# Kernel optimization log

Hardware: AMD Instinct MI355X
Metric: run time of the kernel (lower is better)

## Reference

```python
import jax, jax.numpy as jnp
import numpy as np
from jax.scipy.special import logsumexp

L, B, C, H = 1024, 256, 96, 768
STD = (1.0 / C) ** 0.5


def setup_inputs() -> dict:
    key = jax.random.key(0)
    ks = jax.random.split(key, 8)
    emit = jax.random.normal(ks[0], (L, B, C), dtype=jnp.float32)
    hidden = jax.random.normal(ks[1], (B, H), dtype=jnp.float32)
    target = jax.random.randint(ks[2], (L, B), 0, C)
    # variable sentence lengths in [L//2, L]; mask[0] is always True
    lens = jax.random.randint(ks[3], (B,), L // 2, L + 1)
    mask = jnp.arange(L)[:, None] < lens[None, :]
    Wt = jax.random.normal(ks[4], (C * C, H), dtype=jnp.float32) * STD
    bt = jnp.zeros((C * C,), dtype=jnp.float32)
    Ws = jax.random.normal(ks[5], (C, H), dtype=jnp.float32) * STD
    bs = jnp.zeros((C,), dtype=jnp.float32)
    We = jax.random.normal(ks[6], (C, H), dtype=jnp.float32) * STD
    be = jnp.zeros((C,), dtype=jnp.float32)
    return {"emit": emit, "hidden": hidden, "target": target, "mask": mask,
            "Wt": Wt, "bt": bt, "Ws": Ws, "bs": bs, "We": We, "be": be}


def _crf_loss(emit, hidden, target, mask, Wt, bt, Ws, bs, We, be):
    l, b, c = emit.shape
    trans = (hidden @ Wt.T + bt).reshape(b, c, c)          # [B, prev, next]
    t_start = hidden @ Ws.T + bs                           # [B, C]
    t_end = hidden @ We.T + be                             # [B, C]

    # ---- log partition (forward algorithm), sequential scan over time ----
    def step(log_alpha, xs):
        emit_i, mask_i = xs                                # [B,C], [B]
        # scores[b,p,n] = log_alpha[b,p] + trans[b,p,n] + emit_i[b,n]
        new = logsumexp(log_alpha[:, :, None] + trans + emit_i[:, None, :], axis=1)
        log_alpha = jnp.where(mask_i[:, None], new, log_alpha)
        return log_alpha, None

    log_alpha0 = emit[0] + t_start
    log_alpha, _ = jax.lax.scan(step, log_alpha0, (emit[1:], mask[1:]))
    log_z = logsumexp(log_alpha + t_end, axis=1).sum()

    # ---- gold path score ----
    bidx = jnp.arange(b)
    tr_sc = trans[bidx[None, :], target[:-1], target[1:]]          # [L-1, B]
    emit_sc = jnp.take_along_axis(emit, target[:, :, None], axis=2)[:, :, 0]  # [L, B]
    scores = emit_sc.at[1:].add(tr_sc)
    score = jnp.sum(scores * mask.astype(emit.dtype))
    ends = mask.sum(axis=0) - 1                                    # [B]
    last_tag = target[ends, bidx]
    score = score + t_start[bidx, target[0]].sum() + t_end[bidx, last_tag].sum()

    return (log_z - score) / b


def reference(emit, hidden, target, mask, Wt, bt, Ws, bs, We, be):
    return _crf_loss(emit, hidden, target, mask, Wt, bt, Ws, bs, We, be)
```

## Files before the change

### kernel.cpp

```cpp
#include <hip/hip_runtime.h>
#include <hip/hip_bf16.h>
#include <stdint.h>

#define LL 1024
#define BB 256
#define CC 96
#define HH 768
#define NW 9216
#define NTOT 9408
#define SEGS 8
#define SEGLEN 128
#define CHPB 15

typedef __attribute__((ext_vector_type(4))) float floatx4;
typedef __attribute__((ext_vector_type(2))) float floatx2;
typedef __attribute__((ext_vector_type(8))) short short8;

#define KAPPA 0x1p-16f
#define NEG_LOG_KAPPA 11.090354888959125f

__device__ __forceinline__ unsigned short f2bf(float f) {
  uint32_t u = __float_as_uint(f);
  return (unsigned short)((u + 0x7FFFu + ((u >> 16) & 1u)) >> 16);
}

#define GA_LD 40

__global__ __launch_bounds__(256) void gemm_mfma(
    const float* __restrict__ hidden, const float* __restrict__ Wt,
    const float* __restrict__ Ws, const float* __restrict__ We,
    const float* __restrict__ bt, const float* __restrict__ bs,
    const float* __restrict__ be, float* __restrict__ trans,
    float* __restrict__ tstart, float* __restrict__ tend) {
  __shared__ __align__(16) unsigned short As[128 * GA_LD];
  __shared__ __align__(16) unsigned short Bs[128 * GA_LD];
  const int t = threadIdx.x;
  const int lane = t & 63, wid = t >> 6;
  const int wm = wid >> 1, wn = wid & 1;
  const int l15 = lane & 15, qd = lane >> 4;
  const int m0 = blockIdx.y * 128, n0 = blockIdx.x * 128;
  const int srow = t >> 1, shalf = t & 1;

  floatx4 acc[4][4];
#pragma unroll
  for (int i = 0; i < 4; ++i)
#pragma unroll
    for (int j = 0; j < 4; ++j) acc[i][j] = (floatx4){0.f, 0.f, 0.f, 0.f};

  const int r = n0 + srow;
  const float* bsrc = (r < NW)        ? Wt + (size_t)r * HH
                      : (r < NW + CC) ? Ws + (size_t)(r - NW) * HH
                      : (r < NTOT)    ? We + (size_t)(r - NW - CC) * HH
                                      : nullptr;
  const float* asrc = hidden + (size_t)(m0 + srow) * HH;
  const int sidx = srow * GA_LD + shalf * 16;

  for (int k0 = 0; k0 < HH; k0 += 32) {
    __syncthreads();
    {
      const float4* s4 = (const float4*)(asrc + k0 + shalf * 16);
      uint32_t w[8];
#pragma unroll
      for (int u = 0; u < 4; ++u) {
        float4 v = s4[u];
        w[2 * u] = (uint32_t)f2bf(v.x) | ((uint32_t)f2bf(v.y) << 16);
        w[2 * u + 1] = (uint32_t)f2bf(v.z) | ((uint32_t)f2bf(v.w) << 16);
      }
      *(uint4*)&As[sidx] = make_uint4(w[0], w[1], w[2], w[3]);
      *(uint4*)&As[sidx + 8] = make_uint4(w[4], w[5], w[6], w[7]);
    }
    {
      uint32_t w[8];
      if (bsrc) {
        const float4* s4 = (const float4*)(bsrc + k0 + shalf * 16);
#pragma unroll
        for (int u = 0; u < 4; ++u) {
          float4 v = s4[u];
          w[2 * u] = (uint32_t)f2bf(v.x) | ((uint32_t)f2bf(v.y) << 16);
          w[2 * u + 1] = (uint32_t)f2bf(v.z) | ((uint32_t)f2bf(v.w) << 16);
        }
      } else {
#pragma unroll
        for (int u = 0; u < 8; ++u) w[u] = 0u;
      }
      *(uint4*)&Bs[sidx] = make_uint4(w[0], w[1], w[2], w[3]);
      *(uint4*)&Bs[sidx + 8] = make_uint4(w[4], w[5], w[6], w[7]);
    }
    __syncthreads();
    short8 af[4], bf[4];
#pragma unroll
    for (int i = 0; i < 4; ++i)
      af[i] = *(const short8*)&As[(64 * wm + 16 * i + l15) * GA_LD + qd * 8];
#pragma unroll
    for (int j = 0; j < 4; ++j)
      bf[j] = *(const short8*)&Bs[(64 * wn + 16 * j + l15) * GA_LD + qd * 8];
#pragma unroll
    for (int i = 0; i < 4; ++i)
#pragma unroll
      for (int j = 0; j < 4; ++j)
        acc[i][j] = __builtin_amdgcn_mfma_f32_16x16x32_bf16(af[i], bf[j],
                                                            acc[i][j], 0, 0, 0);
  }

#pragma unroll
  for (int j = 0; j < 4; ++j) {
    int n = n0 + 64 * wn + 16 * j + l15;
    if (n >= NTOT) continue;
    float bv;
    float* dst;
    int ldo;
    if (n < NW) {
      bv = bt[n]; dst = trans + n; ldo = NW;
    } else if (n < NW + CC) {
      bv = bs[n - NW]; dst = tstart + (n - NW); ldo = CC;
    } else {
      bv = be[n - NW - CC]; dst = tend + (n - NW - CC); ldo = CC;
    }
#pragma unroll
    for (int i = 0; i < 4; ++i)
#pragma unroll
      for (int rr = 0; rr < 4; ++rr) {
        int m = m0 + 64 * wm + 16 * i + 4 * qd + rr;
        dst[(size_t)m * ldo] = acc[i][j][rr] + bv;
      }
  }
}

__device__ __forceinline__ float wredf(float v) {
#pragma unroll
  for (int m = 32; m >= 1; m >>= 1) v += __shfl_xor(v, m);
  return v;
}
__device__ __forceinline__ int wredi(int v) {
#pragma unroll
  for (int m = 32; m >= 1; m >>= 1) v += __shfl_xor(v, m);
  return v;
}
__device__ __forceinline__ float bcast0(float x) {
  return __uint_as_float(__builtin_amdgcn_readfirstlane(__float_as_uint(x)));
}
__device__ __forceinline__ int get_len(const void* mask, int b, int l) {
  int cnt = 0;
  unsigned w0 = *(const unsigned*)mask;
  if (w0 == 1u) {
    const int* m32 = (const int*)mask;
    for (int i = l; i < LL; i += 64) cnt += (m32[i * BB + b] != 0);
  } else if (w0 == 0x01010101u) {
    const unsigned char* m8 = (const unsigned char*)mask;
    for (int i = l; i < LL; i += 64) cnt += (m8[i * BB + b] != 0);
  } else {
    const float* mf = (const float*)mask;
    for (int i = l; i < LL; i += 64) cnt += (mf[i * BB + b] != 0.f);
  }
  return wredi(cnt);
}

__global__ __launch_bounds__(64, 2) void crf_chain(
    const float* __restrict__ emit, const void* __restrict__ mask,
    const float* __restrict__ trans, const float* __restrict__ tstart,
    float* __restrict__ xvec, float* __restrict__ lsc) {
  const int cid = blockIdx.x;
  const int b = cid / CHPB;
  const int k = cid - CHPB * b;
  const bool isfw = (k < SEGS);
  const int seg = isfw ? k : (k - (SEGS - 1));
  const int l = threadIdx.x;
  const int pr = l >> 1, s = l & 1;

  __shared__ __align__(16) float ebuf[2][8][CC];
  __shared__ __align__(16) float u_lds[CC];

  const int len = get_len(mask, b, l);
  const int lo = seg * SEGLEN + 1;
  const int hi = min((seg + 1) * SEGLEN, len - 1);
  float* xout = xvec + (size_t)cid * CC;
  if (hi < lo) {
    xout[l] = 1.f;
    if (l < 32) xout[l + 64] = 1.f;
    if (l == 0) lsc[cid] = 0.f;
    return;
  }
  const int n = hi - lo + 1;

  const float* tb = trans + (size_t)b * (CC * CC);
  floatx2 T2[3][24];
  if (isfw) {
#pragma unroll
    for (int j = 0; j < 24; ++j) {
      const float* r0 = tb + (48 * s + 2 * j) * CC + 3 * pr;
      const float* r1 = r0 + CC;
#pragma unroll
      for (int o = 0; o < 3; ++o)
        T2[o][j] = (floatx2){__expf(r0[o]), __expf(r1[o])};
    }
  } else {
#pragma unroll
    for (int o = 0; o < 3; ++o) {
      const float* row = tb + (3 * pr + o) * CC + 48 * s;
#pragma unroll
      for (int j = 0; j < 24; ++j)
        T2[o][j] = (floatx2){__expf(row[2 * j]), __expf(row[2 * j + 1])};
    }
  }

  const float4* e4 = (const float4*)emit;
  const int eoff = 3 * pr + 2 * s;
  float L = 0.f, pv = 1.f;

#define STAGE_CHUNK(baserow, slot)                                        \
  {                                                                       \
    _Pragma("unroll") for (int u = 0; u < 3; ++u) {                       \
      int v = l + 64 * u;                                                 \
      int rw = v / 24, c4 = v - 24 * rw;                                  \
      float4 vv = e4[(((baserow) + rw) * BB + b) * 24 + c4];              \
      floatx4 o = {__expf(vv.x) * KAPPA, __expf(vv.y) * KAPPA,            \
                   __expf(vv.z) * KAPPA, __expf(vv.w) * KAPPA};           \
      *(floatx4*)&ebuf[slot][rw][c4 * 4] = o;                             \
    }                                                                     \
  }

#define INNER_DOT(a0, a1, a2)                                             \
  float a0, a1, a2;                                                       \
  {                                                                       \
    const floatx4* up = (const floatx4*)&u_lds[48 * s];                   \
    floatx2 A0 = {0.f, 0.f}, B0 = {0.f, 0.f};                             \
    floatx2 A1 = {0.f, 0.f}, B1 = {0.f, 0.f};                             \
    floatx2 A2 = {0.f, 0.f}, B2 = {0.f, 0.f};                             \
    _Pragma("unroll") for (int j4 = 0; j4 < 12; ++j4) {                   \
      floatx4 U = up[j4];                                                 \
      floatx2 lo2 = {U.x, U.y}, hi2 = {U.z, U.w};                         \
      A0 += lo2 * T2[0][2 * j4]; B0 += hi2 * T2[0][2 * j4 + 1];           \
      A1 += lo2 * T2[1][2 * j4]; B1 += hi2 * T2[1][2 * j4 + 1];           \
      A2 += lo2 * T2[2][2 * j4]; B2 += hi2 * T2[2][2 * j4 + 1];           \
    }                                                                     \
    floatx2 S0 = A0 + B0, S1 = A1 + B1, S2 = A2 + B2;                     \
    a0 = S0.x + S0.y; a1 = S1.x + S1.y; a2 = S2.x + S2.y;                 \
    a0 += __shfl_xor(a0, 1);                                              \
    a1 += __shfl_xor(a1, 1);                                              \
    a2 += __shfl_xor(a2, 1);                                              \
  }

  if (isfw) {
    const int base0 = lo & ~7;
    STAGE_CHUNK(base0, (base0 >> 3) & 1);
    if (seg == 0) {
      float a00 = emit[(size_t)b * CC] + tstart[b * CC];
      L = a00;
      float v = emit[(size_t)b * CC + l] + tstart[b * CC + l];
      u_lds[l] = __expf(v - a00);
      if (l < 32) {
        int c2 = l + 64;
        float v2 = emit[(size_t)b * CC + c2] + tstart[b * CC + c2];
        u_lds[c2] = __expf(v2 - a00);
      }
    } else {
      u_lds[l] = 1.f;
      if (l < 32) u_lds[l + 64] = 1.f;
    }
    asm volatile("" ::: "memory");
    int jj = 1;
    for (int i = lo; i <= hi; ++i, ++jj) {
      if ((i & 7) == 0) {
        STAGE_CHUNK(i, (i >> 3) & 1);
        asm volatile("" ::: "memory");
      }
      float invP = 1.f;
      if ((jj & 3) == 0) { invP = 1.0f / pv; L += __logf(pv); }
      INNER_DOT(a0, a1, a2);
      floatx2 E = *(const floatx2*)&ebuf[(i >> 3) & 1][i & 7][eoff];
      float o0 = a0 * E.x * invP;
      if (((jj + 1) & 3) == 0) pv = bcast0(o0);
      if (s == 0) {
        floatx2 wv = {o0, a1 * E.y * invP};
        *(floatx2*)&u_lds[3 * pr] = wv;
      } else {
        u_lds[3 * pr + 2] = a2 * E.x * invP;
      }
      asm volatile("" ::: "memory");
    }
  } else {
    const int cb = hi & ~7;
    STAGE_CHUNK(cb, (cb >> 3) & 1);
    asm volatile("" ::: "memory");
    u_lds[l] = ebuf[(hi >> 3) & 1][hi & 7][l];
    if (l < 32) u_lds[l + 64] = ebuf[(hi >> 3) & 1][hi & 7][l + 64];
    asm volatile("" ::: "memory");
    int jj = 1;
    for (int i = hi; i >= lo; --i, ++jj) {
      if ((i & 7) == 0 && i > lo) {
        STAGE_CHUNK(i - 8, ((i >> 3) & 1) ^ 1);
        asm volatile("" ::: "memory");
      }
      float invP = 1.f;
      if ((jj & 3) == 0) { invP = 1.0f / pv; L += __logf(pv); }
      INNER_DOT(a0, a1, a2);
      floatx2 E = (i > lo)
          ? *(const floatx2*)&ebuf[((i - 1) >> 3) & 1][(i - 1) & 7][eoff]
          : (floatx2){1.f, 1.f};
      float o0 = a0 * E.x * invP;
      if (((jj + 1) & 3) == 0) pv = bcast0(o0);
      if (s == 0) {
        floatx2 wv = {o0, a1 * E.y * invP};
        *(floatx2*)&u_lds[3 * pr] = wv;
      } else {
        u_lds[3 * pr + 2] = a2 * E.x * invP;
      }
      asm volatile("" ::: "memory");
    }
  }

  asm volatile("" ::: "memory");
  xout[l] = u_lds[l];
  if (l < 32) xout[l + 64] = u_lds[l + 64];
  if (l == 0) lsc[cid] = L + (float)n * NEG_LOG_KAPPA;
}

__global__ __launch_bounds__(64) void crf_compose(
    const float* __restrict__ emit, const int* __restrict__ target,
    const void* __restrict__ mask, const float* __restrict__ trans,
    const float* __restrict__ tstart, const float* __restrict__ tend,
    const float* __restrict__ xvec, const float* __restrict__ lsc,
    float* __restrict__ out) {
  const int b = blockIdx.x;
  const int l = threadIdx.x;
  const int len = get_len(mask, b, l);

  float Lam = lsc[b * CHPB + 0];
  const float* xcur = xvec + (size_t)(b * CHPB + 0) * CC;
  for (int s2 = 1; s2 < SEGS; ++s2) {
    if (s2 * SEGLEN + 1 > len - 1) break;
    const float* bh = xvec + (size_t)(b * CHPB + (SEGS - 1) + s2) * CC;
    const float* ah = xvec + (size_t)(b * CHPB + s2) * CC;
    float pn = bh[l] * xcur[l];
    float pd = bh[l];
    if (l < 32) {
      pn += bh[l + 64] * xcur[l + 64];
      pd += bh[l + 64];
    }
    float num = wredf(pn), den = wredf(pd);
    Lam += __logf(num / den) + lsc[b * CHPB + s2];
    xcur = ah;
  }
  float zp = xcur[l] * __expf(tend[b * CC + l]);
  if (l < 32) zp += xcur[l + 64] * __expf(tend[b * CC + l + 64]);
  float logz = Lam + __logf(wredf(zp));

  const float* tb = trans + (size_t)b * (CC * CC);
  float sc = 0.f;
  for (int i = l; i < len; i += 64) {
    int tg = target[i * BB + b];
    sc += emit[((size_t)i * BB + b) * CC + tg];
    if (i >= 1) sc += tb[target[(i - 1) * BB + b] * CC + tg];
  }
  float score = wredf(sc);
  if (l == 0) {
    score += tstart[b * CC + target[b]] +
             tend[b * CC + target[(len - 1) * BB + b]];
    atomicAdd(out, (logz - score) * (1.0f / 256.0f));
  }
}

extern "C" void kernel_launch(void* const* d_in, const int* in_sizes, int n_in,
                              void* d_out, int out_size, void* d_ws, size_t ws_size,
                              hipStream_t stream) {
  const float* emit = (const float*)d_in[0];
  const float* hidden = (const float*)d_in[1];
  const int* target = (const int*)d_in[2];
  const void* mask = d_in[3];
  const float* Wt = (const float*)d_in[4];
  const float* bt = (const float*)d_in[5];
  const float* Ws = (const float*)d_in[6];
  const float* bs = (const float*)d_in[7];
  const float* We = (const float*)d_in[8];
  const float* be = (const float*)d_in[9];

  float* trans_ws = (float*)d_ws;
  float* ts_ws = trans_ws + (size_t)BB * CC * CC;
  float* te_ws = ts_ws + (size_t)BB * CC;
  float* xvec = te_ws + (size_t)BB * CC;
  float* lsc = xvec + (size_t)BB * CHPB * CC;

  hipMemsetAsync(d_out, 0, sizeof(float), stream);

  gemm_mfma<<<dim3((NTOT + 127) / 128, 2), 256, 0, stream>>>(
      hidden, Wt, Ws, We, bt, bs, be, trans_ws, ts_ws, te_ws);

  crf_chain<<<BB * CHPB, 64, 0, stream>>>(emit, mask, trans_ws, ts_ws, xvec, lsc);

  crf_compose<<<BB, 64, 0, stream>>>(emit, target, mask, trans_ws, ts_ws, te_ws,
                                     xvec, lsc, (float*)d_out);
}
```

Before: 389.6 us.

## Interleave two independent chain segments per wavefront in crf_chain

Each 64-thread block now runs two independent segment recurrences (A and B) in lockstep, sharing the exp-transformed transition registers, so the latency of one segment's dot and LDS round trip can overlap with the other's. The grid drops from 15 blocks per batch row to 8, and launch bounds move from 2 to 1 waves per EU to make room for the extra state. Segments whose length exceeds the shorter partner run in tail loops. The cost is fewer concurrent waves and serial tails when the two segment lengths differ.

```diff
diff --git a/kernel.cpp b/kernel.cpp
--- a/kernel.cpp
+++ b/kernel.cpp
@@ -155,32 +155,55 @@
   return wredi(cnt);
 }
 
-__global__ __launch_bounds__(64, 2) void crf_chain(
+__global__ __launch_bounds__(64, 1) void crf_chain(
     const float* __restrict__ emit, const void* __restrict__ mask,
     const float* __restrict__ trans, const float* __restrict__ tstart,
     float* __restrict__ xvec, float* __restrict__ lsc) {
-  const int cid = blockIdx.x;
-  const int b = cid / CHPB;
-  const int k = cid - CHPB * b;
-  const bool isfw = (k < SEGS);
-  const int seg = isfw ? k : (k - (SEGS - 1));
+  const int blk = blockIdx.x;
+  const int b = blk >> 3;
+  const int k = blk & 7;
+  const bool isfw = (k < 4);
+  int segA, segB;
+  bool hasB;
+  if (isfw) {
+    segA = k; segB = k + 4; hasB = true;
+  } else if (k < 7) {
+    segA = k - 3; segB = k + 1; hasB = true;
+  } else {
+    segA = 4; segB = 0; hasB = false;
+  }
   const int l = threadIdx.x;
   const int pr = l >> 1, s = l & 1;
 
-  __shared__ __align__(16) float ebuf[2][8][CC];
-  __shared__ __align__(16) float u_lds[CC];
+  __shared__ __align__(16) float ebA[2][8][CC];
+  __shared__ __align__(16) float uAv[CC];
+  __shared__ __align__(16) float ebB[2][8][CC];
+  __shared__ __align__(16) float uBv[CC];
 
   const int len = get_len(mask, b, l);
-  const int lo = seg * SEGLEN + 1;
-  const int hi = min((seg + 1) * SEGLEN, len - 1);
-  float* xout = xvec + (size_t)cid * CC;
-  if (hi < lo) {
-    xout[l] = 1.f;
-    if (l < 32) xout[l + 64] = 1.f;
-    if (l == 0) lsc[cid] = 0.f;
+  const int loA = segA * SEGLEN + 1;
+  const int hiA = min((segA + 1) * SEGLEN, len - 1);
+  const int loB = segB * SEGLEN + 1;
+  const int hiB = hasB ? min((segB + 1) * SEGLEN, len - 1) : -1;
+  const int cidA = b * CHPB + (isfw ? segA : 7 + segA);
+  const int cidB = b * CHPB + (isfw ? segB : 7 + segB);
+  const bool actB = hasB && (hiB >= loB);
+  const int nA = hiA - loA + 1;
+  const int nB = actB ? (hiB - loB + 1) : 0;
+
+  if (hasB && !actB) {
+    float* xo = xvec + (size_t)cidB * CC;
+    xo[l] = 1.f;
+    if (l < 32) xo[l + 64] = 1.f;
+    if (l == 0) lsc[cidB] = 0.f;
+  }
+  if (hiA < loA) {
+    float* xo = xvec + (size_t)cidA * CC;
+    xo[l] = 1.f;
+    if (l < 32) xo[l + 64] = 1.f;
+    if (l == 0) lsc[cidA] = 0.f;
     return;
   }
-  const int n = hi - lo + 1;
 
   const float* tb = trans + (size_t)b * (CC * CC);
   floatx2 T2[3][24];
@@ -205,114 +228,190 @@
 
   const float4* e4 = (const float4*)emit;
   const int eoff = 3 * pr + 2 * s;
-  float L = 0.f, pv = 1.f;
-
-#define STAGE_CHUNK(baserow, slot)                                        \
-  {                                                                       \
-    _Pragma("unroll") for (int u = 0; u < 3; ++u) {                       \
-      int v = l + 64 * u;                                                 \
-      int rw = v / 24, c4 = v - 24 * rw;                                  \
-      float4 vv = e4[(((baserow) + rw) * BB + b) * 24 + c4];              \
-      floatx4 o = {__expf(vv.x) * KAPPA, __expf(vv.y) * KAPPA,            \
-                   __expf(vv.z) * KAPPA, __expf(vv.w) * KAPPA};           \
-      *(floatx4*)&ebuf[slot][rw][c4 * 4] = o;                             \
-    }                                                                     \
-  }
-
-#define INNER_DOT(a0, a1, a2)                                             \
-  float a0, a1, a2;                                                       \
-  {                                                                       \
-    const floatx4* up = (const floatx4*)&u_lds[48 * s];                   \
-    floatx2 A0 = {0.f, 0.f}, B0 = {0.f, 0.f};                             \
-    floatx2 A1 = {0.f, 0.f}, B1 = {0.f, 0.f};                             \
-    floatx2 A2 = {0.f, 0.f}, B2 = {0.f, 0.f};                             \
-    _Pragma("unroll") for (int j4 = 0; j4 < 12; ++j4) {                   \
-      floatx4 U = up[j4];                                                 \
-      floatx2 lo2 = {U.x, U.y}, hi2 = {U.z, U.w};                         \
-      A0 += lo2 * T2[0][2 * j4]; B0 += hi2 * T2[0][2 * j4 + 1];           \
-      A1 += lo2 * T2[1][2 * j4]; B1 += hi2 * T2[1][2 * j4 + 1];           \
-      A2 += lo2 * T2[2][2 * j4]; B2 += hi2 * T2[2][2 * j4 + 1];           \
-    }                                                                     \
-    floatx2 S0 = A0 + B0, S1 = A1 + B1, S2 = A2 + B2;                     \
-    a0 = S0.x + S0.y; a1 = S1.x + S1.y; a2 = S2.x + S2.y;                 \
-    a0 += __shfl_xor(a0, 1);                                              \
-    a1 += __shfl_xor(a1, 1);                                              \
-    a2 += __shfl_xor(a2, 1);                                              \
-  }
+  float LA = 0.f, pvA = 1.f, LB = 0.f, pvB = 1.f;
+
+#define CLOB asm volatile("" ::: "memory")
+
+  auto STAGE = [&](float (*eb)[8][CC], int baserow, int slot) {
+#pragma unroll
+    for (int uu = 0; uu < 3; ++uu) {
+      int v = l + 64 * uu;
+      int rw = v / 24, c4 = v - 24 * rw;
+      float4 vv = e4[((baserow + rw) * BB + b) * 24 + c4];
+      floatx4 o = {__expf(vv.x) * KAPPA, __expf(vv.y) * KAPPA,
+                   __expf(vv.z) * KAPPA, __expf(vv.w) * KAPPA};
+      *(floatx4*)&eb[slot][rw][c4 * 4] = o;
+    }
+  };
+
+  auto DOT = [&](const float* ub, float& a0, float& a1, float& a2) {
+    const floatx4* up = (const floatx4*)&ub[48 * s];
+    floatx2 A0 = {0.f, 0.f}, B0 = {0.f, 0.f};
+    floatx2 A1 = {0.f, 0.f}, B1 = {0.f, 0.f};
+    floatx2 A2 = {0.f, 0.f}, B2 = {0.f, 0.f};
+#pragma unroll
+    for (int j4 = 0; j4 < 12; ++j4) {
+      floatx4 U = up[j4];
+      floatx2 lo2 = {U.x, U.y}, hi2 = {U.z, U.w};
+      A0 += lo2 * T2[0][2 * j4]; B0 += hi2 * T2[0][2 * j4 + 1];
+      A1 += lo2 * T2[1][2 * j4]; B1 += hi2 * T2[1][2 * j4 + 1];
+      A2 += lo2 * T2[2][2 * j4]; B2 += hi2 * T2[2][2 * j4 + 1];
+    }
+    floatx2 S0 = A0 + B0, S1 = A1 + B1, S2 = A2 + B2;
+    a0 = S0.x + S0.y; a1 = S1.x + S1.y; a2 = S2.x + S2.y;
+    a0 += __shfl_xor(a0, 1);
+    a1 += __shfl_xor(a1, 1);
+    a2 += __shfl_xor(a2, 1);
+  };
+
+  auto STEPF = [&](int i, int jjv, float& pvv, float& Lv,
+                   float (*eb)[8][CC], float* ub) {
+    float invP = 1.f;
+    if ((jjv & 3) == 0) { invP = 1.0f / pvv; Lv += __logf(pvv); }
+    float a0, a1, a2;
+    DOT(ub, a0, a1, a2);
+    floatx2 E = *(const floatx2*)&eb[(i >> 3) & 1][i & 7][eoff];
+    float o0 = a0 * E.x * invP;
+    if (((jjv + 1) & 3) == 0) pvv = bcast0(o0);
+    if (s == 0) {
+      floatx2 wv = {o0, a1 * E.y * invP};
+      *(floatx2*)&ub[3 * pr] = wv;
+    } else {
+      ub[3 * pr + 2] = a2 * E.x * invP;
+    }
+  };
+
+  auto STEPB = [&](int i, int lo, int jjv, float& pvv, float& Lv,
+                   float (*eb)[8][CC], float* ub) {
+    float invP = 1.f;
+    if ((jjv & 3) == 0) { invP = 1.0f / pvv; Lv += __logf(pvv); }
+    float a0, a1, a2;
+    DOT(ub, a0, a1, a2);
+    floatx2 E = (i > lo)
+        ? *(const floatx2*)&eb[((i - 1) >> 3) & 1][(i - 1) & 7][eoff]
+        : (floatx2){1.f, 1.f};
+    float o0 = a0 * E.x * invP;
+    if (((jjv + 1) & 3) == 0) pvv = bcast0(o0);
+    if (s == 0) {
+      floatx2 wv = {o0, a1 * E.y * invP};
+      *(floatx2*)&ub[3 * pr] = wv;
+    } else {
+      ub[3 * pr + 2] = a2 * E.x * invP;
+    }
+  };
 
   if (isfw) {
-    const int base0 = lo & ~7;
-    STAGE_CHUNK(base0, (base0 >> 3) & 1);
-    if (seg == 0) {
+    const int bA0 = loA & ~7;
+    STAGE(ebA, bA0, (bA0 >> 3) & 1);
+    if (actB) {
+      const int bB0 = loB & ~7;
+      STAGE(ebB, bB0, (bB0 >> 3) & 1);
+    }
+    if (segA == 0) {
       float a00 = emit[(size_t)b * CC] + tstart[b * CC];
-      L = a00;
+      LA = a00;
       float v = emit[(size_t)b * CC + l] + tstart[b * CC + l];
-      u_lds[l] = __expf(v - a00);
+      uAv[l] = __expf(v - a00);
       if (l < 32) {
         int c2 = l + 64;
         float v2 = emit[(size_t)b * CC + c2] + tstart[b * CC + c2];
-        u_lds[c2] = __expf(v2 - a00);
+        uAv[c2] = __expf(v2 - a00);
       }
     } else {
-      u_lds[l] = 1.f;
-      if (l < 32) u_lds[l + 64] = 1.f;
-    }
-    asm volatile("" ::: "memory");
+      uAv[l] = 1.f;
+      if (l < 32) uAv[l + 64] = 1.f;
+    }
+    if (actB) {
+      uBv[l] = 1.f;
+      if (l < 32) uBv[l + 64] = 1.f;
+    }
+    CLOB;
     int jj = 1;
-    for (int i = lo; i <= hi; ++i, ++jj) {
-      if ((i & 7) == 0) {
-        STAGE_CHUNK(i, (i >> 3) & 1);
-        asm volatile("" ::: "memory");
-      }
-      float invP = 1.f;
-      if ((jj & 3) == 0) { invP = 1.0f / pv; L += __logf(pv); }
-      INNER_DOT(a0, a1, a2);
-      floatx2 E = *(const floatx2*)&ebuf[(i >> 3) & 1][i & 7][eoff];
-      float o0 = a0 * E.x * invP;
-      if (((jj + 1) & 3) == 0) pv = bcast0(o0);
-      if (s == 0) {
-        floatx2 wv = {o0, a1 * E.y * invP};
-        *(floatx2*)&u_lds[3 * pr] = wv;
-      } else {
-        u_lds[3 * pr + 2] = a2 * E.x * invP;
-      }
-      asm volatile("" ::: "memory");
+    int iA = loA, iB = loB;
+    const int nmin = actB ? min(nA, nB) : 0;
+    for (; jj <= nmin; ++jj, ++iA, ++iB) {
+      bool st = false;
+      if ((iA & 7) == 0) { STAGE(ebA, iA, (iA >> 3) & 1); st = true; }
+      if ((iB & 7) == 0) { STAGE(ebB, iB, (iB >> 3) & 1); st = true; }
+      if (st) CLOB;
+      STEPF(iA, jj, pvA, LA, ebA, uAv);
+      STEPF(iB, jj, pvB, LB, ebB, uBv);
+      CLOB;
+    }
+    int jjA = jj;
+    for (; iA <= hiA; ++iA, ++jjA) {
+      if ((iA & 7) == 0) { STAGE(ebA, iA, (iA >> 3) & 1); CLOB; }
+      STEPF(iA, jjA, pvA, LA, ebA, uAv);
+      CLOB;
+    }
+    int jjB = jj;
+    for (; actB && iB <= hiB; ++iB, ++jjB) {
+      if ((iB & 7) == 0) { STAGE(ebB, iB, (iB >> 3) & 1); CLOB; }
+      STEPF(iB, jjB, pvB, LB, ebB, uBv);
+      CLOB;
     }
   } else {
-    const int cb = hi & ~7;
-    STAGE_CHUNK(cb, (cb >> 3) & 1);
-    asm volatile("" ::: "memory");
-    u_lds[l] = ebuf[(hi >> 3) & 1][hi & 7][l];
-    if (l < 32) u_lds[l + 64] = ebuf[(hi >> 3) & 1][hi & 7][l + 64];
-    asm volatile("" ::: "memory");
+    const int cA0 = hiA & ~7;
+    STAGE(ebA, cA0, (cA0 >> 3) & 1);
+    if (actB) {
+      const int cB0 = hiB & ~7;
+      STAGE(ebB, cB0, (cB0 >> 3) & 1);
+    }
+    CLOB;
+    uAv[l] = ebA[(hiA >> 3) & 1][hiA & 7][l];
+    if (l < 32) uAv[l + 64] = ebA[(hiA >> 3) & 1][hiA & 7][l + 64];
+    if (actB) {
+      uBv[l] = ebB[(hiB >> 3) & 1][hiB & 7][l];
+      if (l < 32) uBv[l + 64] = ebB[(hiB >> 3) & 1][hiB & 7][l + 64];
+    }
+    CLOB;
     int jj = 1;
-    for (int i = hi; i >= lo; --i, ++jj) {
-      if ((i & 7) == 0 && i > lo) {
-        STAGE_CHUNK(i - 8, ((i >> 3) & 1) ^ 1);
-        asm volatile("" ::: "memory");
-      }
-      float invP = 1.f;
-      if ((jj & 3) == 0) { invP = 1.0f / pv; L += __logf(pv); }
-      INNER_DOT(a0, a1, a2);
-      floatx2 E = (i > lo)
-          ? *(const floatx2*)&ebuf[((i - 1) >> 3) & 1][(i - 1) & 7][eoff]
-          : (floatx2){1.f, 1.f};
-      float o0 = a0 * E.x * invP;
-      if (((jj + 1) & 3) == 0) pv = bcast0(o0);
-      if (s == 0) {
-        floatx2 wv = {o0, a1 * E.y * invP};
-        *(floatx2*)&u_lds[3 * pr] = wv;
-      } else {
-        u_lds[3 * pr + 2] = a2 * E.x * invP;
-      }
-      asm volatile("" ::: "memory");
-    }
-  }
-
-  asm volatile("" ::: "memory");
-  xout[l] = u_lds[l];
-  if (l < 32) xout[l + 64] = u_lds[l + 64];
-  if (l == 0) lsc[cid] = L + (float)n * NEG_LOG_KAPPA;
+    int iA = hiA, iB = hiB;
+    const int nmin = actB ? min(nA, nB) : 0;
+    for (; jj <= nmin; ++jj, --iA, --iB) {
+      bool st = false;
+      if ((iA & 7) == 0 && iA > loA) {
+        STAGE(ebA, iA - 8, ((iA >> 3) & 1) ^ 1); st = true;
+      }
+      if ((iB & 7) == 0 && iB > loB) {
+        STAGE(ebB, iB - 8, ((iB >> 3) & 1) ^ 1); st = true;
+      }
+      if (st) CLOB;
+      STEPB(iA, loA, jj, pvA, LA, ebA, uAv);
+      STEPB(iB, loB, jj, pvB, LB, ebB, uBv);
+      CLOB;
+    }
+    int jjA = jj;
+    for (; iA >= loA; --iA, ++jjA) {
+      if ((iA & 7) == 0 && iA > loA) {
+        STAGE(ebA, iA - 8, ((iA >> 3) & 1) ^ 1); CLOB;
+      }
+      STEPB(iA, loA, jjA, pvA, LA, ebA, uAv);
+      CLOB;
+    }
+    int jjB = jj;
+    for (; actB && iB >= loB; --iB, ++jjB) {
+      if ((iB & 7) == 0 && iB > loB) {
+        STAGE(ebB, iB - 8, ((iB >> 3) & 1) ^ 1); CLOB;
+      }
+      STEPB(iB, loB, jjB, pvB, LB, ebB, uBv);
+      CLOB;
+    }
+  }
+
+  CLOB;
+  {
+    float* xo = xvec + (size_t)cidA * CC;
+    xo[l] = uAv[l];
+    if (l < 32) xo[l + 64] = uAv[l + 64];
+    if (l == 0) lsc[cidA] = LA + (float)nA * NEG_LOG_KAPPA;
+  }
+  if (actB) {
+    float* xo = xvec + (size_t)cidB * CC;
+    xo[l] = uBv[l];
+    if (l < 32) xo[l + 64] = uBv[l + 64];
+    if (l == 0) lsc[cidB] = LB + (float)nB * NEG_LOG_KAPPA;
+  }
 }
 
 __global__ __launch_bounds__(64) void crf_compose(
@@ -385,7 +484,7 @@
   gemm_mfma<<<dim3((NTOT + 127) / 128, 2), 256, 0, stream>>>(
       hidden, Wt, Ws, We, bt, bs, be, trans_ws, ts_ws, te_ws);
 
-  crf_chain<<<BB * CHPB, 64, 0, stream>>>(emit, mask, trans_ws, ts_ws, xvec, lsc);
+  crf_chain<<<BB * 8, 64, 0, stream>>>(emit, mask, trans_ws, ts_ws, xvec, lsc);
 
   crf_compose<<<BB, 64, 0, stream>>>(emit, target, mask, trans_ws, ts_ws, te_ws,
                                      xvec, lsc, (float*)d_out);
```

After: 442.3 us. +13.5%, slower.

## Split CRF chain matvec across lane quads with DPP reductions instead of pairs

Applied to the files above, without the earlier changes.

Each lane now owns 6 output tags over a quarter of the previous-tag dimension (24 entries) instead of 3 tags over half (48). Partial sums are combined within a quad using DPP moves rather than a single shfl_xor. This halves the LDS vector reads per step and swaps ds_swizzle/bpermute shuffles for cheaper DPP ops. In exchange it adds a second reduction stage per output and leaves lane q=3 idle on writes.

```diff
diff --git a/kernel.cpp b/kernel.cpp
--- a/kernel.cpp
+++ b/kernel.cpp
@@ -139,6 +139,11 @@
 __device__ __forceinline__ float bcast0(float x) {
   return __uint_as_float(__builtin_amdgcn_readfirstlane(__float_as_uint(x)));
 }
+__device__ __forceinline__ float qsum4(float x) {
+  x += __int_as_float(__builtin_amdgcn_mov_dpp(__float_as_int(x), 0xB1, 0xF, 0xF, false));
+  x += __int_as_float(__builtin_amdgcn_mov_dpp(__float_as_int(x), 0x4E, 0xF, 0xF, false));
+  return x;
+}
 __device__ __forceinline__ int get_len(const void* mask, int b, int l) {
   int cnt = 0;
   unsigned w0 = *(const unsigned*)mask;
@@ -165,7 +170,7 @@
   const bool isfw = (k < SEGS);
   const int seg = isfw ? k : (k - (SEGS - 1));
   const int l = threadIdx.x;
-  const int pr = l >> 1, s = l & 1;
+  const int g = l >> 2, q = l & 3;
 
   __shared__ __align__(16) float ebuf[2][8][CC];
   __shared__ __align__(16) float u_lds[CC];
@@ -183,28 +188,27 @@
   const int n = hi - lo + 1;
 
   const float* tb = trans + (size_t)b * (CC * CC);
-  floatx2 T2[3][24];
+  floatx2 T2[6][12];
   if (isfw) {
 #pragma unroll
-    for (int j = 0; j < 24; ++j) {
-      const float* r0 = tb + (48 * s + 2 * j) * CC + 3 * pr;
-      const float* r1 = r0 + CC;
-#pragma unroll
-      for (int o = 0; o < 3; ++o)
-        T2[o][j] = (floatx2){__expf(r0[o]), __expf(r1[o])};
-    }
+    for (int t = 0; t < 6; ++t)
+#pragma unroll
+      for (int m = 0; m < 12; ++m) {
+        const float* p0 = tb + (24 * q + 2 * m) * CC + 6 * g + t;
+        T2[t][m] = (floatx2){__expf(p0[0]), __expf(p0[CC])};
+      }
   } else {
 #pragma unroll
-    for (int o = 0; o < 3; ++o) {
-      const float* row = tb + (3 * pr + o) * CC + 48 * s;
-#pragma unroll
-      for (int j = 0; j < 24; ++j)
-        T2[o][j] = (floatx2){__expf(row[2 * j]), __expf(row[2 * j + 1])};
+    for (int t = 0; t < 6; ++t) {
+      const float* row = tb + (6 * g + t) * CC + 24 * q;
+#pragma unroll
+      for (int m = 0; m < 12; ++m)
+        T2[t][m] = (floatx2){__expf(row[2 * m]), __expf(row[2 * m + 1])};
     }
   }
 
   const float4* e4 = (const float4*)emit;
-  const int eoff = 3 * pr + 2 * s;
+  const int eidx = 6 * g + 2 * (q < 3 ? q : 2);
   float L = 0.f, pv = 1.f;
 
 #define STAGE_CHUNK(baserow, slot)                                        \
@@ -219,25 +223,43 @@
     }                                                                     \
   }
 
-#define INNER_DOT(a0, a1, a2)                                             \
-  float a0, a1, a2;                                                       \
+#define INNER_DOT6(a0_, a1_, a2_, a3_, a4_, a5_)                          \
+  float a0_, a1_, a2_, a3_, a4_, a5_;                                     \
   {                                                                       \
-    const floatx4* up = (const floatx4*)&u_lds[48 * s];                   \
-    floatx2 A0 = {0.f, 0.f}, B0 = {0.f, 0.f};                             \
-    floatx2 A1 = {0.f, 0.f}, B1 = {0.f, 0.f};                             \
-    floatx2 A2 = {0.f, 0.f}, B2 = {0.f, 0.f};                             \
-    _Pragma("unroll") for (int j4 = 0; j4 < 12; ++j4) {                   \
-      floatx4 U = up[j4];                                                 \
+    const floatx4* up = (const floatx4*)&u_lds[24 * q];                   \
+    floatx2 A0 = {0.f, 0.f}, A1 = {0.f, 0.f}, A2 = {0.f, 0.f};            \
+    floatx2 A3 = {0.f, 0.f}, A4 = {0.f, 0.f}, A5 = {0.f, 0.f};            \
+    floatx2 B0 = {0.f, 0.f}, B1 = {0.f, 0.f}, B2 = {0.f, 0.f};            \
+    floatx2 B3 = {0.f, 0.f}, B4 = {0.f, 0.f}, B5 = {0.f, 0.f};            \
+    _Pragma("unroll") for (int nn = 0; nn < 6; ++nn) {                    \
+      floatx4 U = up[nn];                                                 \
       floatx2 lo2 = {U.x, U.y}, hi2 = {U.z, U.w};                         \
-      A0 += lo2 * T2[0][2 * j4]; B0 += hi2 * T2[0][2 * j4 + 1];           \
-      A1 += lo2 * T2[1][2 * j4]; B1 += hi2 * T2[1][2 * j4 + 1];           \
-      A2 += lo2 * T2[2][2 * j4]; B2 += hi2 * T2[2][2 * j4 + 1];           \
+      A0 += lo2 * T2[0][2 * nn]; B0 += hi2 * T2[0][2 * nn + 1];           \
+      A1 += lo2 * T2[1][2 * nn]; B1 += hi2 * T2[1][2 * nn + 1];           \
+      A2 += lo2 * T2[2][2 * nn]; B2 += hi2 * T2[2][2 * nn + 1];           \
+      A3 += lo2 * T2[3][2 * nn]; B3 += hi2 * T2[3][2 * nn + 1];           \
+      A4 += lo2 * T2[4][2 * nn]; B4 += hi2 * T2[4][2 * nn + 1];           \
+      A5 += lo2 * T2[5][2 * nn]; B5 += hi2 * T2[5][2 * nn + 1];           \
     }                                                                     \
-    floatx2 S0 = A0 + B0, S1 = A1 + B1, S2 = A2 + B2;                     \
-    a0 = S0.x + S0.y; a1 = S1.x + S1.y; a2 = S2.x + S2.y;                 \
-    a0 += __shfl_xor(a0, 1);                                              \
-    a1 += __shfl_xor(a1, 1);                                              \
-    a2 += __shfl_xor(a2, 1);                                              \
+    floatx2 S;                                                            \
+    S = A0 + B0; a0_ = S.x + S.y;                                         \
+    S = A1 + B1; a1_ = S.x + S.y;                                         \
+    S = A2 + B2; a2_ = S.x + S.y;                                         \
+    S = A3 + B3; a3_ = S.x + S.y;                                         \
+    S = A4 + B4; a4_ = S.x + S.y;                                         \
+    S = A5 + B5; a5_ = S.x + S.y;                                         \
+    a0_ = qsum4(a0_); a1_ = qsum4(a1_); a2_ = qsum4(a2_);                 \
+    a3_ = qsum4(a3_); a4_ = qsum4(a4_); a5_ = qsum4(a5_);                 \
+  }
+
+#define WRITE_U(a0_, a1_, a2_, a3_, a4_, a5_, Ex_, Ey_, invP_)            \
+  {                                                                       \
+    float wx = (q == 0) ? a0_ : ((q == 1) ? a2_ : a4_);                   \
+    float wy = (q == 0) ? a1_ : ((q == 1) ? a3_ : a5_);                   \
+    if (q < 3) {                                                          \
+      floatx2 wv = {wx * (Ex_) * (invP_), wy * (Ey_) * (invP_)};          \
+      *(floatx2*)&u_lds[6 * g + 2 * q] = wv;                              \
+    }                                                                     \
   }
 
   if (isfw) {
@@ -266,16 +288,11 @@
       }
       float invP = 1.f;
       if ((jj & 3) == 0) { invP = 1.0f / pv; L += __logf(pv); }
-      INNER_DOT(a0, a1, a2);
-      floatx2 E = *(const floatx2*)&ebuf[(i >> 3) & 1][i & 7][eoff];
+      INNER_DOT6(a0, a1, a2, a3, a4, a5);
+      floatx2 E = *(const floatx2*)&ebuf[(i >> 3) & 1][i & 7][eidx];
       float o0 = a0 * E.x * invP;
       if (((jj + 1) & 3) == 0) pv = bcast0(o0);
-      if (s == 0) {
-        floatx2 wv = {o0, a1 * E.y * invP};
-        *(floatx2*)&u_lds[3 * pr] = wv;
-      } else {
-        u_lds[3 * pr + 2] = a2 * E.x * invP;
-      }
+      WRITE_U(a0, a1, a2, a3, a4, a5, E.x, E.y, invP);
       asm volatile("" ::: "memory");
     }
   } else {
@@ -293,18 +310,13 @@
       }
       float invP = 1.f;
       if ((jj & 3) == 0) { invP = 1.0f / pv; L += __logf(pv); }
-      INNER_DOT(a0, a1, a2);
+      INNER_DOT6(a0, a1, a2, a3, a4, a5);
       floatx2 E = (i > lo)
-          ? *(const floatx2*)&ebuf[((i - 1) >> 3) & 1][(i - 1) & 7][eoff]
+          ? *(const floatx2*)&ebuf[((i - 1) >> 3) & 1][(i - 1) & 7][eidx]
           : (floatx2){1.f, 1.f};
       float o0 = a0 * E.x * invP;
       if (((jj + 1) & 3) == 0) pv = bcast0(o0);
-      if (s == 0) {
-        floatx2 wv = {o0, a1 * E.y * invP};
-        *(floatx2*)&u_lds[3 * pr] = wv;
-      } else {
-        u_lds[3 * pr + 2] = a2 * E.x * invP;
-      }
+      WRITE_U(a0, a1, a2, a3, a4, a5, E.x, E.y, invP);
       asm volatile("" ::: "memory");
     }
   }
```

Result: no change. 393.8 us (+1.1%).
